# Kernel tuning notes

Hardware: AMD Instinct MI355X
Metric: run time of the kernel (lower is better)

## Reference

```python
import jax, jax.numpy as jnp
import numpy as np

N = 100000       # nodes
E = 1600000      # edges
NFEAT = 256
NHID = 128
NCLASS = 1


def setup_inputs() -> dict:
    key = jax.random.key(0)
    ks = jax.random.split(key, 9)
    x = jax.random.normal(ks[0], (N, NFEAT), dtype=jnp.float32)
    src = jax.random.randint(ks[1], (E,), 0, N, dtype=jnp.int32)
    dst = jax.random.randint(ks[2], (E,), 0, N, dtype=jnp.int32)
    W1 = jax.random.normal(ks[3], (NFEAT, NHID), dtype=jnp.float32) * (1.0 / np.sqrt(NFEAT))
    b1 = jnp.zeros((NHID,), dtype=jnp.float32)
    W2 = jax.random.normal(ks[4], (NHID, NHID), dtype=jnp.float32) * (1.0 / np.sqrt(NHID))
    b2 = jnp.zeros((NHID,), dtype=jnp.float32)
    Wfc = jax.random.normal(ks[5], (NHID, NCLASS), dtype=jnp.float32) * (1.0 / np.sqrt(NHID))
    bfc = jnp.zeros((NCLASS,), dtype=jnp.float32)
    return {"x": x, "W1": W1, "b1": b1, "W2": W2, "b2": b2,
            "Wfc": Wfc, "bfc": bfc, "src": src, "dst": dst}


def reference(x, W1, b1, W2, b2, Wfc, bfc, src, dst):
    # Symmetric GCN normalization (DGL GraphConv, norm='both').
    ones = jnp.ones((E,), dtype=jnp.float32)
    out_deg = jax.ops.segment_sum(ones, src, num_segments=N)
    in_deg = jax.ops.segment_sum(ones, dst, num_segments=N)
    norm_s = jnp.maximum(out_deg, 1.0) ** -0.5  # [N] src-side norm
    norm_d = jnp.maximum(in_deg, 1.0) ** -0.5   # [N] dst-side norm

    def gconv(h, W, b):
        # weight-before-aggregate (math-equivalent; minimizes [E, d] gather width)
        m = (h * norm_s[:, None]) @ W          # [N, out]
        agg = jax.ops.segment_sum(m[src], dst, num_segments=N)  # SpMM via gather+scatter-add
        return agg * norm_d[:, None] + b

    h1 = jax.nn.relu(gconv(x, W1, b1))
    # dropout is identity in eval mode
    h2 = gconv(h1, W2, b2)
    return h2 @ Wfc + bfc  # [N, NCLASS]
```

## Files before the change

### kernel.cpp

```cpp
#include <hip/hip_runtime.h>
#include <hip/hip_bf16.h>

#define NNODES 100000
#define NEDGES 1600000
#define NF 256
#define NH 128
#define SCAN_ELEMS 1024
#define SCAN_NBLK ((NNODES + SCAN_ELEMS - 1) / SCAN_ELEMS)

#define HG 200
#define HCHUNK (NEDGES / HG)
#define HBINS 50000
#define HR 2
#define HWORDS (NNODES / 2)

#define WPREP_BLOCKS 129

typedef _Float16 half4v __attribute__((ext_vector_type(4)));
typedef _Float16 half8v __attribute__((ext_vector_type(8)));
typedef float floatx16 __attribute__((ext_vector_type(16)));

__device__ __forceinline__ int pos16(int k) {
    return (((k >> 2) & 1) << 3) + (k & 3) + (((k >> 3) & 1) << 2);
}
__device__ __forceinline__ int ipos16(int p) {
    int g = (p >> 3) & 1, j = p & 7;
    return g * 4 + (j & 3) + ((j >> 2) << 3);
}

__device__ __forceinline__ float2 h2f2(unsigned u) {
    union { unsigned u; _Float16 h[2]; } c; c.u = u;
    return make_float2((float)c.h[0], (float)c.h[1]);
}

__device__ __forceinline__ void load_lds16(const void* g, void* l) {
    __builtin_amdgcn_global_load_lds(
        (const __attribute__((address_space(1))) void*)g,
        (__attribute__((address_space(3))) void*)l, 16, 0, 0);
}

__global__ __launch_bounds__(512)
void hist_part_kernel(const int* __restrict__ src, const int* __restrict__ dst,
                      unsigned* __restrict__ partial) {
    __shared__ unsigned lds[HBINS / 2];
    const int g = blockIdx.x, t = threadIdx.x;
    const int e0 = g * HCHUNK;
    for (int r = 0; r < HR; ++r) {
        const int lo = r * HBINS;
        for (int i = t; i < HBINS / 2; i += 512) lds[i] = 0;
        __syncthreads();
        for (int i = t; i < HCHUNK; i += 512) {
            unsigned us = (unsigned)(src[e0 + i] - lo);
            if (us < HBINS) atomicAdd(&lds[us >> 1], 1u << ((us & 1) * 16));
            unsigned ud = (unsigned)(dst[e0 + i] - lo);
            if (ud < HBINS) atomicAdd(&lds[ud >> 1], 1u << ((ud & 1) * 16 + 8));
        }
        __syncthreads();
        unsigned* dp = partial + (size_t)g * HWORDS + (lo >> 1);
        for (int i = t; i < HBINS / 2; i += 512) dp[i] = lds[i];
        __syncthreads();
    }
}

__global__ __launch_bounds__(256)
void degscan_kernel(const unsigned* __restrict__ partial,
                    unsigned char* __restrict__ offb,
                    float* __restrict__ ns, float* __restrict__ nd,
                    int* __restrict__ cnt_in) {
    int w = blockIdx.x * 256 + threadIdx.x;
    if (w >= HWORDS) return;
    unsigned o0 = 0, i0 = 0, o1 = 0, i1 = 0;
    for (int g0 = 0; g0 < HG; g0 += 8) {
        unsigned v[8];
        #pragma unroll
        for (int j = 0; j < 8; ++j) v[j] = partial[(size_t)(g0 + j) * HWORDS + w];
        #pragma unroll
        for (int j = 0; j < 8; ++j) {
            *(unsigned short*)(offb + (size_t)(g0 + j) * NNODES + 2 * w) =
                (unsigned short)((i0 & 0xffu) | ((i1 & 0xffu) << 8));
            o0 += v[j] & 0xffu;         i0 += (v[j] >> 8) & 0xffu;
            o1 += (v[j] >> 16) & 0xffu; i1 += v[j] >> 24;
        }
    }
    int n0 = 2 * w, n1 = 2 * w + 1;
    ns[n0] = rsqrtf((float)max((int)o0, 1));
    nd[n0] = rsqrtf((float)max((int)i0, 1));
    cnt_in[n0] = (int)i0;
    ns[n1] = rsqrtf((float)max((int)o1, 1));
    nd[n1] = rsqrtf((float)max((int)i1, 1));
    cnt_in[n1] = (int)i1;
}

__global__ __launch_bounds__(256)
void scanA_kernel(const int* __restrict__ cnt, int* __restrict__ pre,
                  int* __restrict__ bsum, int n) {
    __shared__ int tsum[256];
    int b = blockIdx.x, t = threadIdx.x;
    int base = b * SCAN_ELEMS + t * 4;
    int v[4]; int s = 0;
    #pragma unroll
    for (int k = 0; k < 4; ++k) { int idx = base + k; v[k] = (idx < n) ? cnt[idx] : 0; s += v[k]; }
    tsum[t] = s;
    __syncthreads();
    for (int off = 1; off < 256; off <<= 1) {
        int val = (t >= off) ? tsum[t - off] : 0;
        __syncthreads();
        tsum[t] += val;
        __syncthreads();
    }
    int run = (t == 0) ? 0 : tsum[t - 1];
    #pragma unroll
    for (int k = 0; k < 4; ++k) { int idx = base + k; if (idx < n) pre[idx] = run; run += v[k]; }
    if (t == 255) bsum[b] = tsum[255];
}

__global__ __launch_bounds__(128)
void scanB_kernel(int* __restrict__ bsum, int nb, int* __restrict__ row_ptr) {
    __shared__ int s[128];
    int t = threadIdx.x;
    int v = (t < nb) ? bsum[t] : 0;
    s[t] = v;
    __syncthreads();
    for (int off = 1; off < 128; off <<= 1) {
        int u = (t >= off) ? s[t - off] : 0;
        __syncthreads();
        s[t] += u;
        __syncthreads();
    }
    if (t < nb) bsum[t] = s[t] - v;
    if (t == 0) row_ptr[NNODES] = NEDGES;
}

__global__ __launch_bounds__(256)
void scanC_kernel(int* __restrict__ pre, const int* __restrict__ bsum, int n) {
    int add = bsum[blockIdx.x];
    int base = blockIdx.x * SCAN_ELEMS + threadIdx.x;
    #pragma unroll
    for (int k = 0; k < 4; ++k) {
        int idx = base + k * 256;
        if (idx < n) pre[idx] += add;
    }
}

__global__ __launch_bounds__(512)
void fill_kernel(const int* __restrict__ src, const int* __restrict__ dst,
                 const int* __restrict__ row_ptr, const unsigned char* __restrict__ offb,
                 int* __restrict__ col) {
    __shared__ unsigned lcur[HBINS / 2];
    const int g = blockIdx.x, t = threadIdx.x;
    const int e0 = g * HCHUNK;
    const unsigned char* ob = offb + (size_t)g * NNODES;
    for (int r = 0; r < HR; ++r) {
        const int lo = r * HBINS;
        for (int i = t; i < HBINS / 2; i += 512) lcur[i] = 0;
        __syncthreads();
        for (int i = t; i < HCHUNK; i += 512) {
            int d = dst[e0 + i];
            unsigned ud = (unsigned)(d - lo);
            if (ud < HBINS) {
                unsigned prev = atomicAdd(&lcur[ud >> 1], 1u << ((ud & 1) * 16));
                unsigned rank = (prev >> ((ud & 1) * 16)) & 0xffffu;
                int p = row_ptr[d] + (int)ob[d] + (int)rank;
                col[p] = src[e0 + i];
            }
        }
        __syncthreads();
    }
}

__global__ __launch_bounds__(256)
void prep_w_kernel(const float* __restrict__ W1, const float* __restrict__ b1,
                   _Float16* __restrict__ Wt1, float* __restrict__ b1p,
                   const float* __restrict__ W2, const float* __restrict__ Wfc,
                   const float* __restrict__ b2, const float* __restrict__ bfc,
                   float* __restrict__ v2p, float* __restrict__ c0) {
    int b = blockIdx.x, t = threadIdx.x;
    if (b < WPREP_BLOCKS) {
        int id = b * 256 + t;
        if (id < NF * NH) {
            int k = id >> 7, n = id & 127;
            Wt1[(size_t)n * NF + (k & ~15) + pos16(k & 15)] = (_Float16)W1[id];
        } else if (id < NF * NH + NH) {
            int pos = id - NF * NH;
            int k = (pos & ~15) + ipos16(pos & 15);
            b1p[pos] = b1[k];
        }
    } else {
        if (t < 128) {
            float s = 0.f;
            #pragma unroll 16
            for (int j = 0; j < 128; ++j) s += W2[t * 128 + j] * Wfc[j];
            v2p[(t & ~15) + pos16(t & 15)] = s;
        } else if (t < 192) {
            int lane = t - 128;
            float c = b2[lane] * Wfc[lane] + b2[lane + 64] * Wfc[lane + 64];
            #pragma unroll
            for (int off = 32; off > 0; off >>= 1) c += __shfl_down(c, off);
            if (lane == 0) c0[0] = c + bfc[0];
        }
    }
}

__global__ __launch_bounds__(256, 4)
void gemm1_kernel(const float* __restrict__ X, const _Float16* __restrict__ Wt,
                  const float* __restrict__ norm_s, _Float16* __restrict__ Cout,
                  int N) {
    __shared__ __align__(16) float As[128 * 64];
    const int tid = threadIdx.x;
    const int l = tid & 63, w = tid >> 6;
    const int wr = w >> 1, wc = w & 1;
    const int row0 = blockIdx.x * 128;
    const int s0 = blockIdx.x & 3;

    const _Float16* Bb = Wt + (size_t)(wc * 64 + (l & 31)) * NF + (l >> 5) * 8;
    const int ar = wr * 64 + (l & 31);
    const int swz = ar & 7;
    const int g = l >> 5;
    const int lr = l >> 4, lc = l & 15;
    floatx16 acc[2][2] = {};

    for (int ii = 0; ii < 4; ++ii) {
        const int step = (s0 + ii) & 3;
        #pragma unroll
        for (int i = 0; i < 8; ++i) {
            int R = w * 32 + i * 4;
            int r = R + lr;
            int grow = row0 + r;
            int srcc = lc ^ (r & 7);
            if (grow < N)
                load_lds16(X + (size_t)grow * NF + step * 64 + srcc * 4,
                           &As[(size_t)R * 64]);
        }
        __syncthreads();
        #pragma unroll
        for (int kk = 0; kk < 4; ++kk) {
            int ca = kk * 4 + g;
            int cb = ca + 2;
            float4 a0l = *(const float4*)&As[(size_t)ar * 64 + (ca ^ swz) * 4];
            float4 a0h = *(const float4*)&As[(size_t)ar * 64 + (cb ^ swz) * 4];
            float4 a1l = *(const float4*)&As[(size_t)(ar + 32) * 64 + (ca ^ swz) * 4];
            float4 a1h = *(const float4*)&As[(size_t)(ar + 32) * 64 + (cb ^ swz) * 4];
            half8v a0 = { (_Float16)a0l.x, (_Float16)a0l.y, (_Float16)a0l.z, (_Float16)a0l.w,
                          (_Float16)a0h.x, (_Float16)a0h.y, (_Float16)a0h.z, (_Float16)a0h.w };
            half8v a1 = { (_Float16)a1l.x, (_Float16)a1l.y, (_Float16)a1l.z, (_Float16)a1l.w,
                          (_Float16)a1h.x, (_Float16)a1h.y, (_Float16)a1h.z, (_Float16)a1h.w };
            const _Float16* bp = Bb + (step * 4 + kk) * 16;
            half8v b0 = *(const half8v*)bp;
            half8v b1 = *(const half8v*)(bp + (size_t)32 * NF);
            acc[0][0] = __builtin_amdgcn_mfma_f32_32x32x16_f16(a0, b0, acc[0][0], 0, 0, 0);
            acc[0][1] = __builtin_amdgcn_mfma_f32_32x32x16_f16(a0, b1, acc[0][1], 0, 0, 0);
            acc[1][0] = __builtin_amdgcn_mfma_f32_32x32x16_f16(a1, b0, acc[1][0], 0, 0, 0);
            acc[1][1] = __builtin_amdgcn_mfma_f32_32x32x16_f16(a1, b1, acc[1][1], 0, 0, 0);
        }
        __syncthreads();
    }

    const int cpos = pos16(l & 15);
    const int chi = ((l >> 4) & 1) << 4;
    #pragma unroll
    for (int m = 0; m < 2; ++m) {
        #pragma unroll
        for (int r = 0; r < 16; ++r) {
            int rloc = wr * 64 + m * 32 + (r & 3) + ((r >> 2) << 3) + ((l >> 5) << 2);
            int grow = row0 + rloc;
            if (grow < N) {
                float s = norm_s[grow];
                #pragma unroll
                for (int n = 0; n < 2; ++n) {
                    int colbase = wc * 64 + n * 32 + chi;
                    Cout[(size_t)grow * NH + colbase + cpos] = (_Float16)(acc[m][n][r] * s);
                }
            }
        }
    }
}

__global__ __launch_bounds__(512)
void gatherz_kernel(const _Float16* __restrict__ m, const int* __restrict__ row_ptr,
                    const int* __restrict__ col, const float* __restrict__ norm_d,
                    const float* __restrict__ norm_s, const float* __restrict__ b1p,
                    const float* __restrict__ v2p, float* __restrict__ z, int N) {
    int w = (blockIdx.x * 512 + threadIdx.x) >> 6;
    int lane = threadIdx.x & 63;
    if (w >= N) return;
    int beg = __builtin_amdgcn_readfirstlane(row_ptr[w]);
    int end = __builtin_amdgcn_readfirstlane(row_ptr[w + 1]);
    const unsigned* mu = (const unsigned*)m + lane;
    float ax = 0.f, ay = 0.f;
    int i = beg;
    for (; i + 15 < end; i += 16) {
        unsigned u[16];
        #pragma unroll
        for (int j = 0; j < 16; ++j) u[j] = mu[(size_t)col[i + j] * 64];
        #pragma unroll
        for (int j = 0; j < 16; ++j) { float2 v = h2f2(u[j]); ax += v.x; ay += v.y; }
    }
    for (; i + 3 < end; i += 4) {
        unsigned u[4];
        #pragma unroll
        for (int j = 0; j < 4; ++j) u[j] = mu[(size_t)col[i + j] * 64];
        #pragma unroll
        for (int j = 0; j < 4; ++j) { float2 v = h2f2(u[j]); ax += v.x; ay += v.y; }
    }
    for (; i < end; ++i) {
        float2 v = h2f2(mu[(size_t)col[i] * 64]);
        ax += v.x; ay += v.y;
    }
    float nd = norm_d[w], ns = norm_s[w];
    float2 bv = ((const float2*)b1p)[lane];
    float hx = fmaxf(fmaf(ax, nd, bv.x), 0.f) * ns;
    float hy = fmaxf(fmaf(ay, nd, bv.y), 0.f) * ns;
    float2 w2 = ((const float2*)v2p)[lane];
    float p = fmaf(hx, w2.x, hy * w2.y);
    #pragma unroll
    for (int off = 32; off > 0; off >>= 1) p += __shfl_down(p, off);
    if (lane == 0) z[w] = p;
}

__global__ __launch_bounds__(256)
void outsum_kernel(const float* __restrict__ z, const int* __restrict__ row_ptr,
                   const int* __restrict__ col, const float* __restrict__ norm_d,
                   const float* __restrict__ c0, float* __restrict__ out, int N) {
    int w = blockIdx.x * 256 + threadIdx.x;
    if (w >= N) return;
    int beg = row_ptr[w], end = row_ptr[w + 1];
    float s0 = 0.f, s1 = 0.f, s2 = 0.f, s3 = 0.f;
    int i = beg;
    for (; i + 3 < end; i += 4) {
        s0 += z[col[i]];     s1 += z[col[i + 1]];
        s2 += z[col[i + 2]]; s3 += z[col[i + 3]];
    }
    for (; i < end; ++i) s0 += z[col[i]];
    out[w] = norm_d[w] * ((s0 + s1) + (s2 + s3)) + c0[0];
}

extern "C" void kernel_launch(void* const* d_in, const int* in_sizes, int n_in,
                              void* d_out, int out_size, void* d_ws, size_t ws_size,
                              hipStream_t stream) {
    const float* x   = (const float*)d_in[0];
    const float* W1  = (const float*)d_in[1];
    const float* b1  = (const float*)d_in[2];
    const float* W2  = (const float*)d_in[3];
    const float* b2  = (const float*)d_in[4];
    const float* Wfc = (const float*)d_in[5];
    const float* bfc = (const float*)d_in[6];
    const int*   src = (const int*)d_in[7];
    const int*   dst = (const int*)d_in[8];
    float* out = (float*)d_out;

    const int N = NNODES, E = NEDGES;

    char* p = (char*)d_ws;
    float*    norm_s = (float*)p;      p += (size_t)N * 4;
    float*    norm_d = (float*)p;      p += (size_t)N * 4;
    _Float16* bufA_h = (_Float16*)p;   p += (size_t)N * NH * 2;
    _Float16* Wt1    = (_Float16*)p;   p += (size_t)NF * NH * 2;
    float*    b1p    = (float*)p;      p += NH * 4;
    float*    v2p    = (float*)p;      p += NH * 4;
    float*    c0     = (float*)p;      p += 16;
    float*    z      = (float*)p;      p += (size_t)N * 4;
    int*      cnt_in = (int*)p;        p += (size_t)N * 4;
    int*      row_ptr= (int*)p;        p += (size_t)(N + 1) * 4 + 12;
    int*      col    = (int*)p;        p += (size_t)E * 4;
    int*      bsum   = (int*)p;        p += 128 * 4;
    unsigned* partial= (unsigned*)p;
    unsigned char* offb = (unsigned char*)bufA_h;

    hist_part_kernel<<<HG, 512, 0, stream>>>(src, dst, partial);
    degscan_kernel<<<(HWORDS + 255) / 256, 256, 0, stream>>>(partial, offb, norm_s, norm_d, cnt_in);
    scanA_kernel<<<SCAN_NBLK, 256, 0, stream>>>(cnt_in, row_ptr, bsum, N);
    scanB_kernel<<<1, 128, 0, stream>>>(bsum, SCAN_NBLK, row_ptr);
    scanC_kernel<<<SCAN_NBLK, 256, 0, stream>>>(row_ptr, bsum, N);
    fill_kernel<<<HG, 512, 0, stream>>>(src, dst, row_ptr, offb, col);
    prep_w_kernel<<<WPREP_BLOCKS + 1, 256, 0, stream>>>(W1, b1, Wt1, b1p,
                                                        W2, Wfc, b2, bfc, v2p, c0);

    gemm1_kernel<<<(N + 127) / 128, 256, 0, stream>>>(x, Wt1, norm_s, bufA_h, N);
    gatherz_kernel<<<((size_t)N * 64 + 511) / 512, 512, 0, stream>>>(
        bufA_h, row_ptr, col, norm_d, norm_s, b1p, v2p, z, N);
    outsum_kernel<<<(N + 255) / 256, 256, 0, stream>>>(z, row_ptr, col, norm_d, c0, out, N);
}
```

Baseline: 198.8 us.

## Double-buffer X tiles in gemm1 with explicit vmcnt waits

Splits the K loop of gemm1 into 8 steps of 32 columns with two LDS buffers. The next tile's global-to-LDS loads are issued before computing the current one, and a manual s_waitcnt plus raw s_barrier replaces __syncthreads. The aim is to overlap global loads of X with MFMA work instead of stalling on each 64-column stage. Out-of-range row loads are now clamped rather than skipped, and the per-block staggered K start order is dropped. The B-operand loads from global are also counted by vmcnt, so the wait count assumption may be fragile.

New measurement: 197.3 us. Within noise of the previous version (-0.7%).

```diff
diff --git a/kernel.cpp b/kernel.cpp
--- a/kernel.cpp
+++ b/kernel.cpp
@@ -205,46 +205,62 @@
 void gemm1_kernel(const float* __restrict__ X, const _Float16* __restrict__ Wt,
                   const float* __restrict__ norm_s, _Float16* __restrict__ Cout,
                   int N) {
-    __shared__ __align__(16) float As[128 * 64];
+    __shared__ __align__(16) float As[2][128 * 32];
     const int tid = threadIdx.x;
     const int l = tid & 63, w = tid >> 6;
     const int wr = w >> 1, wc = w & 1;
     const int row0 = blockIdx.x * 128;
-    const int s0 = blockIdx.x & 3;
 
     const _Float16* Bb = Wt + (size_t)(wc * 64 + (l & 31)) * NF + (l >> 5) * 8;
     const int ar = wr * 64 + (l & 31);
     const int swz = ar & 7;
     const int g = l >> 5;
-    const int lr = l >> 4, lc = l & 15;
+    const int lr = l >> 3, lc = l & 7;
     floatx16 acc[2][2] = {};
 
-    for (int ii = 0; ii < 4; ++ii) {
-        const int step = (s0 + ii) & 3;
-        #pragma unroll
-        for (int i = 0; i < 8; ++i) {
-            int R = w * 32 + i * 4;
-            int r = R + lr;
-            int grow = row0 + r;
-            int srcc = lc ^ (r & 7);
-            if (grow < N)
-                load_lds16(X + (size_t)grow * NF + step * 64 + srcc * 4,
-                           &As[(size_t)R * 64]);
-        }
-        __syncthreads();
-        #pragma unroll
-        for (int kk = 0; kk < 4; ++kk) {
+    #pragma unroll
+    for (int i = 0; i < 4; ++i) {
+        int R = w * 32 + i * 8;
+        int r = R + lr;
+        int grow = min(row0 + r, N - 1);
+        int srcc = lc ^ (r & 7);
+        load_lds16(X + (size_t)grow * NF + srcc * 4, &As[0][R * 32]);
+    }
+
+    for (int t = 0; t < 8; ++t) {
+        const int cur = t & 1;
+        if (t < 7) {
+            #pragma unroll
+            for (int i = 0; i < 4; ++i) {
+                int R = w * 32 + i * 8;
+                int r = R + lr;
+                int grow = min(row0 + r, N - 1);
+                int srcc = lc ^ (r & 7);
+                load_lds16(X + (size_t)grow * NF + (t + 1) * 32 + srcc * 4,
+                           &As[cur ^ 1][R * 32]);
+            }
+            __builtin_amdgcn_sched_barrier(0);
+            asm volatile("s_waitcnt vmcnt(4)" ::: "memory");
+            __builtin_amdgcn_sched_barrier(0);
+        } else {
+            __builtin_amdgcn_sched_barrier(0);
+            asm volatile("s_waitcnt vmcnt(0)" ::: "memory");
+            __builtin_amdgcn_sched_barrier(0);
+        }
+        __builtin_amdgcn_s_barrier();
+        #pragma unroll
+        for (int kk = 0; kk < 2; ++kk) {
             int ca = kk * 4 + g;
             int cb = ca + 2;
-            float4 a0l = *(const float4*)&As[(size_t)ar * 64 + (ca ^ swz) * 4];
-            float4 a0h = *(const float4*)&As[(size_t)ar * 64 + (cb ^ swz) * 4];
-            float4 a1l = *(const float4*)&As[(size_t)(ar + 32) * 64 + (ca ^ swz) * 4];
-            float4 a1h = *(const float4*)&As[(size_t)(ar + 32) * 64 + (cb ^ swz) * 4];
+            float4 a0l = *(const float4*)&As[cur][(size_t)ar * 32 + (ca ^ swz) * 4];
+            float4 a0h = *(const float4*)&As[cur][(size_t)ar * 32 + (cb ^ swz) * 4];
+            float4 a1l = *(const float4*)&As[cur][(size_t)(ar + 32) * 32 + (ca ^ swz) * 4];
+            float4 a1h = *(const float4*)&As[cur][(size_t)(ar + 32) * 32 + (cb ^ swz) * 4];
             half8v a0 = { (_Float16)a0l.x, (_Float16)a0l.y, (_Float16)a0l.z, (_Float16)a0l.w,
                           (_Float16)a0h.x, (_Float16)a0h.y, (_Float16)a0h.z, (_Float16)a0h.w };
             half8v a1 = { (_Float16)a1l.x, (_Float16)a1l.y, (_Float16)a1l.z, (_Float16)a1l.w,
                           (_Float16)a1h.x, (_Float16)a1h.y, (_Float16)a1h.z, (_Float16)a1h.w };
-            const _Float16* bp = Bb + (step * 4 + kk) * 16;
+            const _Float16* bp = Bb + (t * 2 + kk) * 16;
             half8v b0 = *(const half8v*)bp;
             half8v b1 = *(const half8v*)(bp + (size_t)32 * NF);
             acc[0][0] = __builtin_amdgcn_mfma_f32_32x32x16_f16(a0, b0, acc[0][0], 0, 0, 0);
@@ -252,7 +268,7 @@
             acc[1][0] = __builtin_amdgcn_mfma_f32_32x32x16_f16(a1, b0, acc[1][0], 0, 0, 0);
             acc[1][1] = __builtin_amdgcn_mfma_f32_32x32x16_f16(a1, b1, acc[1][1], 0, 0, 0);
         }
-        __syncthreads();
+        __builtin_amdgcn_s_barrier();
     }
 
     const int cpos = pos16(l & 15);
```
